# Kernel optimization log

Measured on AMD Instinct MI355X. Metric: run time of the kernel, lower is better.

Reference implementation:

```python
import jax, jax.numpy as jnp
import numpy as np

E = 262144      # number of edges (triples)
D = 256         # embed_dim
DOUT = 256      # embed_out_dim
NQ = 65536      # num_query (output nodes)
NK = 65536      # num_key
ALPHA = 0.2     # leaky relu slope
EPS = 1e-12


def setup_inputs() -> dict:
    key = jax.random.key(0)
    ks = jax.random.split(key, 7)
    return {
        "key_list": jax.random.randint(ks[0], (E,), 0, NK),
        "key_embed": jax.random.normal(ks[1], (E, D), jnp.float32),
        "query_list": jax.random.randint(ks[2], (E,), 0, NQ),
        "query_embed": jax.random.normal(ks[3], (E, D), jnp.float32),
        # learned parameters (xavier-ish scale)
        "a": jax.random.normal(ks[4], (DOUT, 2 * D), jnp.float32) * 0.05,
        "a_2": jax.random.normal(ks[5], (1, DOUT), jnp.float32) * 0.05,
        "trans": jax.random.normal(ks[6], (DOUT, D), jnp.float32) * 0.05,
    }


def reference(key_list, key_embed, query_list, query_embed, a, a_2, trans):
    # edge_associated_set = trans @ key_embed.T, kept as (E, DOUT)
    edge_assoc = key_embed @ trans.T                              # (E, DOUT)
    # edge_m = a @ cat(key, query).T, kept as (E, DOUT)
    edge_h = jnp.concatenate([key_embed, query_embed], axis=1)    # (E, 2D)
    edge_m = edge_h @ a.T                                         # (E, DOUT)
    powers = -jax.nn.leaky_relu(edge_m @ a_2[0], negative_slope=ALPHA)  # (E,)
    edge_e = jnp.exp(powers)                                      # (E,) unnormalized attn
    # sparse COO sum over key dim == segment-sum by query index
    e_rowsum = jax.ops.segment_sum(edge_e, query_list, num_segments=NQ)[:, None]  # (NQ,1)
    e_rowsum = jnp.where(e_rowsum == 0.0, EPS, e_rowsum)
    # dropout p=0.0 (eval) -> identity
    edge_w = edge_e[:, None] * edge_assoc                         # (E, DOUT)
    h_prime = jax.ops.segment_sum(edge_w, query_list, num_segments=NQ)  # (NQ, DOUT)
    h_prime = h_prime / e_rowsum
    return jax.nn.elu(h_prime)  # concat=True branch
```

## Files before the change

### kernel.cpp

```cpp
#include <hip/hip_runtime.h>
#include <hip/hip_bf16.h>
#include <math.h>

namespace {
constexpr int kD = 256;
constexpr int kDOUT = 256;
constexpr int kNQ = 65536;
constexpr int kE = 262144;
constexpr float kAlpha = 0.2f;
constexpr float kEps = 1e-12f;
constexpr int kCap = 16;
constexpr int kOvfMax = 4096;
}

typedef short bf16x8 __attribute__((ext_vector_type(8)));
typedef float f32x4 __attribute__((ext_vector_type(4)));
typedef unsigned short u16x8 __attribute__((ext_vector_type(8)));

__global__ void compute_c_kernel(const float* __restrict__ a,
                                 const float* __restrict__ a2,
                                 float* __restrict__ c) {
  const int j = blockIdx.x * blockDim.x + threadIdx.x;
  float s = 0.f;
#pragma unroll 8
  for (int k = 0; k < kDOUT; ++k) s = fmaf(a[k * (2 * kD) + j], a2[k], s);
  c[j] = s;
}

__global__ void zero_kernel(int4* __restrict__ p, int* __restrict__ ovf_n) {
  p[blockIdx.x * 256 + threadIdx.x] = int4{0, 0, 0, 0};
  if (blockIdx.x == 0 && threadIdx.x == 0) *ovf_n = 0;
}

__global__ void cvt_trans_kernel(const float* __restrict__ t, ushort* __restrict__ tb) {
  const int i = blockIdx.x * 256 + threadIdx.x;
  const float4 v = reinterpret_cast<const float4*>(t)[i];
  union { ushort4 u; __hip_bfloat16 h[4]; } p;
  p.h[0] = __float2bfloat16(v.x);
  p.h[1] = __float2bfloat16(v.y);
  p.h[2] = __float2bfloat16(v.z);
  p.h[3] = __float2bfloat16(v.w);
  reinterpret_cast<ushort4*>(tb)[i] = p.u;
}

__global__ __launch_bounds__(256) void qdot_bin_kernel(
    const float* __restrict__ query_embed,
    const int* __restrict__ qlist,
    const float* __restrict__ c,
    int* __restrict__ count,
    int2* __restrict__ bins,
    int* __restrict__ ovf_n,
    int* __restrict__ ovf_q,
    int* __restrict__ ovf_e,
    float* __restrict__ ovf_qd) {
  const int wid = threadIdx.x >> 6;
  const int lane = threadIdx.x & 63;
  const int g = lane >> 4;
  const int l4 = lane & 15;
  const int edge = blockIdx.x * 16 + wid * 4 + g;

  int q = 0;
  if (l4 == 0) q = qlist[edge];

  const float4* qr = reinterpret_cast<const float4*>(query_embed) + (size_t)edge * 64 + l4 * 4;
  const float4 r0 = qr[0], r1 = qr[1], r2 = qr[2], r3 = qr[3];
  const float4 c0 = reinterpret_cast<const float4*>(c)[64 + l4 * 4 + 0];
  const float4 c1 = reinterpret_cast<const float4*>(c)[64 + l4 * 4 + 1];
  const float4 c2 = reinterpret_cast<const float4*>(c)[64 + l4 * 4 + 2];
  const float4 c3 = reinterpret_cast<const float4*>(c)[64 + l4 * 4 + 3];

  float s = r0.x * c0.x + r0.y * c0.y + r0.z * c0.z + r0.w * c0.w
          + r1.x * c1.x + r1.y * c1.y + r1.z * c1.z + r1.w * c1.w
          + r2.x * c2.x + r2.y * c2.y + r2.z * c2.z + r2.w * c2.w
          + r3.x * c3.x + r3.y * c3.y + r3.z * c3.z + r3.w * c3.w;
#pragma unroll
  for (int off = 1; off < 16; off <<= 1) s += __shfl_xor(s, off, 64);

  if (l4 == 0) {
    const int slot = atomicAdd(&count[q], 1);
    if (slot < kCap) {
      bins[q * kCap + slot] = make_int2(edge, __float_as_int(s));
    } else {
      const int o = atomicAdd(ovf_n, 1);
      if (o < kOvfMax) { ovf_q[o] = q; ovf_e[o] = edge; ovf_qd[o] = s; }
    }
  }
}

__global__ __launch_bounds__(256) void gather_kernel(
    const float* __restrict__ key_embed,
    const float* __restrict__ c,
    const int2* __restrict__ bins,
    const int* __restrict__ count,
    const int* __restrict__ ovf_n,
    const int* __restrict__ ovf_q,
    const int* __restrict__ ovf_e,
    const float* __restrict__ ovf_qd,
    ushort* __restrict__ accb) {
  const int wid = threadIdx.x >> 6;
  const int lane = threadIdx.x & 63;
  const int g = lane >> 5;
  const int l5 = lane & 31;
  const int q = blockIdx.x * 8 + wid * 2 + g;

  const int cnt = count[q];
  const int cm = min(cnt, kCap);
  const int2 mybin = (l5 < cm) ? bins[q * kCap + l5] : make_int2(0, 0);

  const float4 ck0 = reinterpret_cast<const float4*>(c)[l5 * 2 + 0];
  const float4 ck1 = reinterpret_cast<const float4*>(c)[l5 * 2 + 1];

  float acc[8] = {};
  float rs = 0.f;

  for (int s = 0; s < cm; s += 4) {
    const int kc = min(4, cm - s);
    float4 r[4][2];
    float qd[4];
#pragma unroll
    for (int t = 0; t < 4; ++t) {
      if (t < kc) {
        const int eg = __shfl(mybin.x, (g << 5) + s + t, 64);
        qd[t] = __int_as_float(__shfl(mybin.y, (g << 5) + s + t, 64));
        const float4* row = reinterpret_cast<const float4*>(key_embed) + (size_t)eg * 64 + l5 * 2;
        r[t][0] = row[0];
        r[t][1] = row[1];
      }
    }
#pragma unroll
    for (int t = 0; t < 4; ++t) {
      if (t < kc) {
        float kd = r[t][0].x * ck0.x + r[t][0].y * ck0.y + r[t][0].z * ck0.z + r[t][0].w * ck0.w
                 + r[t][1].x * ck1.x + r[t][1].y * ck1.y + r[t][1].z * ck1.z + r[t][1].w * ck1.w;
#pragma unroll
        for (int off = 1; off < 32; off <<= 1) kd += __shfl_xor(kd, off, 64);
        const float sv = kd + qd[t];
        const float p = (sv > 0.f) ? sv : kAlpha * sv;
        const float ev = __expf(-p);
        acc[0] = fmaf(ev, r[t][0].x, acc[0]);
        acc[1] = fmaf(ev, r[t][0].y, acc[1]);
        acc[2] = fmaf(ev, r[t][0].z, acc[2]);
        acc[3] = fmaf(ev, r[t][0].w, acc[3]);
        acc[4] = fmaf(ev, r[t][1].x, acc[4]);
        acc[5] = fmaf(ev, r[t][1].y, acc[5]);
        acc[6] = fmaf(ev, r[t][1].z, acc[6]);
        acc[7] = fmaf(ev, r[t][1].w, acc[7]);
        rs += ev;
      }
    }
  }

  if (cnt > kCap) {
    const int n = min(*ovf_n, kOvfMax);
    for (int i = 0; i < n; ++i) {
      if (ovf_q[i] == q) {
        const float4* row = reinterpret_cast<const float4*>(key_embed) +
                            (size_t)ovf_e[i] * 64 + l5 * 2;
        const float4 r0 = row[0], r1 = row[1];
        float kd = r0.x * ck0.x + r0.y * ck0.y + r0.z * ck0.z + r0.w * ck0.w
                 + r1.x * ck1.x + r1.y * ck1.y + r1.z * ck1.z + r1.w * ck1.w;
#pragma unroll
        for (int off = 1; off < 32; off <<= 1) kd += __shfl_xor(kd, off, 64);
        const float sv = kd + ovf_qd[i];
        const float p = (sv > 0.f) ? sv : kAlpha * sv;
        const float ev = __expf(-p);
        acc[0] = fmaf(ev, r0.x, acc[0]);
        acc[1] = fmaf(ev, r0.y, acc[1]);
        acc[2] = fmaf(ev, r0.z, acc[2]);
        acc[3] = fmaf(ev, r0.w, acc[3]);
        acc[4] = fmaf(ev, r1.x, acc[4]);
        acc[5] = fmaf(ev, r1.y, acc[5]);
        acc[6] = fmaf(ev, r1.z, acc[6]);
        acc[7] = fmaf(ev, r1.w, acc[7]);
        rs += ev;
      }
    }
  }

  const float inv = 1.0f / ((rs == 0.f) ? kEps : rs);
  union { u16x8 u; __hip_bfloat16 h[8]; } pk;
#pragma unroll
  for (int j = 0; j < 8; ++j) pk.h[j] = __float2bfloat16(acc[j] * inv);
  *reinterpret_cast<u16x8*>(accb + (size_t)q * kD + l5 * 8) = pk.u;
}

__global__ __launch_bounds__(256) void out_gemm_mfma_kernel(
    const ushort* __restrict__ A,
    const ushort* __restrict__ B,
    float* __restrict__ out) {
  const int wid = threadIdx.x >> 6;
  const int lane = threadIdx.x & 63;
  const int row0 = (blockIdx.x * 4 + wid) * 16;
  const int m = lane & 15;
  const int kb = (lane >> 4) * 8;

  f32x4 acc[16] = {};

  for (int kt = 0; kt < kD; kt += 32) {
    const bf16x8 af = *reinterpret_cast<const bf16x8*>(&A[(size_t)(row0 + m) * kD + kt + kb]);
#pragma unroll
    for (int nt = 0; nt < 16; ++nt) {
      const bf16x8 bf = *reinterpret_cast<const bf16x8*>(&B[(size_t)(nt * 16 + m) * kD + kt + kb]);
      acc[nt] = __builtin_amdgcn_mfma_f32_16x16x32_bf16(af, bf, acc[nt], 0, 0, 0);
    }
  }

#pragma unroll
  for (int nt = 0; nt < 16; ++nt) {
#pragma unroll
    for (int r = 0; r < 4; ++r) {
      const int row = row0 + (lane >> 4) * 4 + r;
      const int col = nt * 16 + (lane & 15);
      const float x = acc[nt][r];
      out[(size_t)row * kDOUT + col] = (x > 0.f) ? x : expm1f(x);
    }
  }
}

extern "C" void kernel_launch(void* const* d_in, const int* in_sizes, int n_in,
                              void* d_out, int out_size, void* d_ws, size_t ws_size,
                              hipStream_t stream) {
  const float* key_embed = (const float*)d_in[1];
  const int* query_list = (const int*)d_in[2];
  const float* query_embed = (const float*)d_in[3];
  const float* a = (const float*)d_in[4];
  const float* a2 = (const float*)d_in[5];
  const float* trans = (const float*)d_in[6];
  float* out = (float*)d_out;

  float* ws = (float*)d_ws;
  float* c = ws;
  int* count = (int*)(c + 512);
  int2* bins = (int2*)(count + kNQ);
  ushort* accb = (ushort*)(bins + (size_t)kNQ * kCap);
  ushort* transb = accb + (size_t)kNQ * kD;
  int* ovf_n = (int*)(transb + (size_t)kDOUT * kD);
  int* ovf_q = ovf_n + 4;
  int* ovf_e = ovf_q + kOvfMax;
  float* ovf_qd = (float*)(ovf_e + kOvfMax);

  zero_kernel<<<kNQ / 4 / 256, 256, 0, stream>>>((int4*)count, ovf_n);
  compute_c_kernel<<<2, 256, 0, stream>>>(a, a2, c);
  cvt_trans_kernel<<<kDOUT * kD / 4 / 256, 256, 0, stream>>>(trans, transb);
  qdot_bin_kernel<<<kE / 16, 256, 0, stream>>>(query_embed, query_list, c, count,
                                               bins, ovf_n, ovf_q, ovf_e, ovf_qd);
  gather_kernel<<<kNQ / 8, 256, 0, stream>>>(key_embed, c, bins, count, ovf_n,
                                             ovf_q, ovf_e, ovf_qd, accb);
  out_gemm_mfma_kernel<<<kNQ / 64, 256, 0, stream>>>(accb, transb, out);
}
```

Baseline: 223.8 us.

## Fuse gather and output GEMM into one kernel via LDS-staged bf16 tile

```diff
diff --git a/kernel.cpp b/kernel.cpp
--- a/kernel.cpp
+++ b/kernel.cpp
@@ -87,7 +87,7 @@
   }
 }
 
-__global__ __launch_bounds__(256) void gather_kernel(
+__global__ __launch_bounds__(256) void gather_gemm_kernel(
     const float* __restrict__ key_embed,
     const float* __restrict__ c,
     const int2* __restrict__ bins,
@@ -96,55 +96,61 @@
     const int* __restrict__ ovf_q,
     const int* __restrict__ ovf_e,
     const float* __restrict__ ovf_qd,
-    ushort* __restrict__ accb) {
+    const ushort* __restrict__ B,
+    float* __restrict__ out) {
+  __shared__ ushort A_lds[16][264];
   const int wid = threadIdx.x >> 6;
   const int lane = threadIdx.x & 63;
-  const int g = lane >> 5;
-  const int l5 = lane & 31;
-  const int q = blockIdx.x * 8 + wid * 2 + g;
+  const int g = lane >> 4;
+  const int l4 = lane & 15;
+  const int qloc = wid * 4 + g;
+  const int q = blockIdx.x * 16 + qloc;
 
   const int cnt = count[q];
   const int cm = min(cnt, kCap);
-  const int2 mybin = (l5 < cm) ? bins[q * kCap + l5] : make_int2(0, 0);
-
-  const float4 ck0 = reinterpret_cast<const float4*>(c)[l5 * 2 + 0];
-  const float4 ck1 = reinterpret_cast<const float4*>(c)[l5 * 2 + 1];
-
-  float acc[8] = {};
+  const int2 mybin = (l4 < cm) ? bins[q * kCap + l4] : make_int2(0, 0);
+
+  const float4 ck0 = reinterpret_cast<const float4*>(c)[l4 * 4 + 0];
+  const float4 ck1 = reinterpret_cast<const float4*>(c)[l4 * 4 + 1];
+  const float4 ck2 = reinterpret_cast<const float4*>(c)[l4 * 4 + 2];
+  const float4 ck3 = reinterpret_cast<const float4*>(c)[l4 * 4 + 3];
+
+  float acc[16] = {};
   float rs = 0.f;
 
   for (int s = 0; s < cm; s += 4) {
     const int kc = min(4, cm - s);
-    float4 r[4][2];
+    float4 r[4][4];
     float qd[4];
 #pragma unroll
     for (int t = 0; t < 4; ++t) {
       if (t < kc) {
-        const int eg = __shfl(mybin.x, (g << 5) + s + t, 64);
-        qd[t] = __int_as_float(__shfl(mybin.y, (g << 5) + s + t, 64));
-        const float4* row = reinterpret_cast<const float4*>(key_embed) + (size_t)eg * 64 + l5 * 2;
-        r[t][0] = row[0];
-        r[t][1] = row[1];
+        const int eg = __shfl(mybin.x, (g << 4) + s + t, 64);
+        qd[t] = __int_as_float(__shfl(mybin.y, (g << 4) + s + t, 64));
+        const float4* row = reinterpret_cast<const float4*>(key_embed) + (size_t)eg * 64 + l4 * 4;
+#pragma unroll
+        for (int u = 0; u < 4; ++u) r[t][u] = row[u];
       }
     }
 #pragma unroll
     for (int t = 0; t < 4; ++t) {
       if (t < kc) {
         float kd = r[t][0].x * ck0.x + r[t][0].y * ck0.y + r[t][0].z * ck0.z + r[t][0].w * ck0.w
-                 + r[t][1].x * ck1.x + r[t][1].y * ck1.y + r[t][1].z * ck1.z + r[t][1].w * ck1.w;
-#pragma unroll
-        for (int off = 1; off < 32; off <<= 1) kd += __shfl_xor(kd, off, 64);
+                 + r[t][1].x * ck1.x + r[t][1].y * ck1.y + r[t][1].z * ck1.z + r[t][1].w * ck1.w
+                 + r[t][2].x * ck2.x + r[t][2].y * ck2.y + r[t][2].z * ck2.z + r[t][2].w * ck2.w
+                 + r[t][3].x * ck3.x + r[t][3].y * ck3.y + r[t][3].z * ck3.z + r[t][3].w * ck3.w;
+#pragma unroll
+        for (int off = 1; off < 16; off <<= 1) kd += __shfl_xor(kd, off, 64);
         const float sv = kd + qd[t];
         const float p = (sv > 0.f) ? sv : kAlpha * sv;
         const float ev = __expf(-p);
-        acc[0] = fmaf(ev, r[t][0].x, acc[0]);
-        acc[1] = fmaf(ev, r[t][0].y, acc[1]);
-        acc[2] = fmaf(ev, r[t][0].z, acc[2]);
-        acc[3] = fmaf(ev, r[t][0].w, acc[3]);
-        acc[4] = fmaf(ev, r[t][1].x, acc[4]);
-        acc[5] = fmaf(ev, r[t][1].y, acc[5]);
-        acc[6] = fmaf(ev, r[t][1].z, acc[6]);
-        acc[7] = fmaf(ev, r[t][1].w, acc[7]);
+#pragma unroll
+        for (int u = 0; u < 4; ++u) {
+          acc[u * 4 + 0] = fmaf(ev, r[t][u].x, acc[u * 4 + 0]);
+          acc[u * 4 + 1] = fmaf(ev, r[t][u].y, acc[u * 4 + 1]);
+          acc[u * 4 + 2] = fmaf(ev, r[t][u].z, acc[u * 4 + 2]);
+          acc[u * 4 + 3] = fmaf(ev, r[t][u].w, acc[u * 4 + 3]);
+        }
         rs += ev;
       }
     }
@@ -155,64 +161,66 @@
     for (int i = 0; i < n; ++i) {
       if (ovf_q[i] == q) {
         const float4* row = reinterpret_cast<const float4*>(key_embed) +
-                            (size_t)ovf_e[i] * 64 + l5 * 2;
-        const float4 r0 = row[0], r1 = row[1];
-        float kd = r0.x * ck0.x + r0.y * ck0.y + r0.z * ck0.z + r0.w * ck0.w
-                 + r1.x * ck1.x + r1.y * ck1.y + r1.z * ck1.z + r1.w * ck1.w;
-#pragma unroll
-        for (int off = 1; off < 32; off <<= 1) kd += __shfl_xor(kd, off, 64);
+                            (size_t)ovf_e[i] * 64 + l4 * 4;
+        float4 r4[4];
+#pragma unroll
+        for (int u = 0; u < 4; ++u) r4[u] = row[u];
+        float kd = r4[0].x * ck0.x + r4[0].y * ck0.y + r4[0].z * ck0.z + r4[0].w * ck0.w
+                 + r4[1].x * ck1.x + r4[1].y * ck1.y + r4[1].z * ck1.z + r4[1].w * ck1.w
+                 + r4[2].x * ck2.x + r4[2].y * ck2.y + r4[2].z * ck2.z + r4[2].w * ck2.w
+                 + r4[3].x * ck3.x + r4[3].y * ck3.y + r4[3].z * ck3.z + r4[3].w * ck3.w;
+#pragma unroll
+        for (int off = 1; off < 16; off <<= 1) kd += __shfl_xor(kd, off, 64);
         const float sv = kd + ovf_qd[i];
         const float p = (sv > 0.f) ? sv : kAlpha * sv;
         const float ev = __expf(-p);
-        acc[0] = fmaf(ev, r0.x, acc[0]);
-        acc[1] = fmaf(ev, r0.y, acc[1]);
-        acc[2] = fmaf(ev, r0.z, acc[2]);
-        acc[3] = fmaf(ev, r0.w, acc[3]);
-        acc[4] = fmaf(ev, r1.x, acc[4]);
-        acc[5] = fmaf(ev, r1.y, acc[5]);
-        acc[6] = fmaf(ev, r1.z, acc[6]);
-        acc[7] = fmaf(ev, r1.w, acc[7]);
+#pragma unroll
+        for (int u = 0; u < 4; ++u) {
+          acc[u * 4 + 0] = fmaf(ev, r4[u].x, acc[u * 4 + 0]);
+          acc[u * 4 + 1] = fmaf(ev, r4[u].y, acc[u * 4 + 1]);
+          acc[u * 4 + 2] = fmaf(ev, r4[u].z, acc[u * 4 + 2]);
+          acc[u * 4 + 3] = fmaf(ev, r4[u].w, acc[u * 4 + 3]);
+        }
         rs += ev;
       }
     }
   }
 
   const float inv = 1.0f / ((rs == 0.f) ? kEps : rs);
-  union { u16x8 u; __hip_bfloat16 h[8]; } pk;
-#pragma unroll
-  for (int j = 0; j < 8; ++j) pk.h[j] = __float2bfloat16(acc[j] * inv);
-  *reinterpret_cast<u16x8*>(accb + (size_t)q * kD + l5 * 8) = pk.u;
-}
-
-__global__ __launch_bounds__(256) void out_gemm_mfma_kernel(
-    const ushort* __restrict__ A,
-    const ushort* __restrict__ B,
-    float* __restrict__ out) {
-  const int wid = threadIdx.x >> 6;
-  const int lane = threadIdx.x & 63;
-  const int row0 = (blockIdx.x * 4 + wid) * 16;
+  union { u16x8 u; __hip_bfloat16 h[8]; } p0, p1;
+#pragma unroll
+  for (int j = 0; j < 8; ++j) p0.h[j] = __float2bfloat16(acc[j] * inv);
+#pragma unroll
+  for (int j = 0; j < 8; ++j) p1.h[j] = __float2bfloat16(acc[8 + j] * inv);
+  *reinterpret_cast<u16x8*>(&A_lds[qloc][l4 * 16]) = p0.u;
+  *reinterpret_cast<u16x8*>(&A_lds[qloc][l4 * 16 + 8]) = p1.u;
+
+  __syncthreads();
+
   const int m = lane & 15;
   const int kb = (lane >> 4) * 8;
-
-  f32x4 acc[16] = {};
-
+  f32x4 acc2[4] = {};
+
+#pragma unroll
   for (int kt = 0; kt < kD; kt += 32) {
-    const bf16x8 af = *reinterpret_cast<const bf16x8*>(&A[(size_t)(row0 + m) * kD + kt + kb]);
-#pragma unroll
-    for (int nt = 0; nt < 16; ++nt) {
-      const bf16x8 bf = *reinterpret_cast<const bf16x8*>(&B[(size_t)(nt * 16 + m) * kD + kt + kb]);
-      acc[nt] = __builtin_amdgcn_mfma_f32_16x16x32_bf16(af, bf, acc[nt], 0, 0, 0);
-    }
-  }
-
-#pragma unroll
-  for (int nt = 0; nt < 16; ++nt) {
+    const bf16x8 af = *reinterpret_cast<const bf16x8*>(&A_lds[m][kt + kb]);
+#pragma unroll
+    for (int nt = 0; nt < 4; ++nt) {
+      const int ntg = wid * 4 + nt;
+      const bf16x8 bf =
+          *reinterpret_cast<const bf16x8*>(&B[(size_t)(ntg * 16 + m) * kD + kt + kb]);
+      acc2[nt] = __builtin_amdgcn_mfma_f32_16x16x32_bf16(af, bf, acc2[nt], 0, 0, 0);
+    }
+  }
+
+#pragma unroll
+  for (int nt = 0; nt < 4; ++nt) {
+    const int ntg = wid * 4 + nt;
 #pragma unroll
     for (int r = 0; r < 4; ++r) {
-      const int row = row0 + (lane >> 4) * 4 + r;
-      const int col = nt * 16 + (lane & 15);
-      const float x = acc[nt][r];
-      out[(size_t)row * kDOUT + col] = (x > 0.f) ? x : expm1f(x);
+      const int row = blockIdx.x * 16 + (lane >> 4) * 4 + r;
+      const float x = acc2[nt][r];
+      out[(size_t)row * kDOUT + ntg * 16 + m] = (x > 0.f) ? x : expm1f(x);
     }
   }
 }
@@ -232,8 +240,7 @@
   float* c = ws;
   int* count = (int*)(c + 512);
   int2* bins = (int2*)(count + kNQ);
-  ushort* accb = (ushort*)(bins + (size_t)kNQ * kCap);
-  ushort* transb = accb + (size_t)kNQ * kD;
+  ushort* transb = (ushort*)(bins + (size_t)kNQ * kCap);
   int* ovf_n = (int*)(transb + (size_t)kDOUT * kD);
   int* ovf_q = ovf_n + 4;
   int* ovf_e = ovf_q + kOvfMax;
@@ -244,7 +251,6 @@
   cvt_trans_kernel<<<kDOUT * kD / 4 / 256, 256, 0, stream>>>(trans, transb);
   qdot_bin_kernel<<<kE / 16, 256, 0, stream>>>(query_embed, query_list, c, count,
                                                bins, ovf_n, ovf_q, ovf_e, ovf_qd);
-  gather_kernel<<<kNQ / 8, 256, 0, stream>>>(key_embed, c, bins, count, ovf_n,
-                                             ovf_q, ovf_e, ovf_qd, accb);
-  out_gemm_mfma_kernel<<<kNQ / 64, 256, 0, stream>>>(accb, transb, out);
-}
+  gather_gemm_kernel<<<kNQ / 16, 256, 0, stream>>>(key_embed, c, bins, count, ovf_n,
+                                                   ovf_q, ovf_e, ovf_qd, transb, out);
+}
```

After: 213.7 us. 1.05x faster.
